# Kernel tuning notes

Hardware: AMD Instinct MI355X
Metric: run time of the kernel (lower is better)

Reference implementation:

```python
import jax, jax.numpy as jnp
import numpy as np

EPS = 1e-5   # BatchNorm3d eps
SLOPE = 0.01 # LeakyReLU default negative_slope

def conv3(x, w, pad):
    return jax.lax.conv_general_dilated(
        x, w, (1, 1, 1), [(pad, pad)] * 3,
        dimension_numbers=('NCDHW', 'OIDHW', 'NCDHW'))

def bn(x):
    # BatchNorm3d in training mode with affine init (weight=1, bias=0):
    # normalize by per-channel batch statistics (biased variance).
    m = x.mean(axis=(0, 2, 3, 4), keepdims=True)
    v = x.var(axis=(0, 2, 3, 4), keepdims=True)
    return (x - m) / jnp.sqrt(v + EPS)

def lrelu(x):
    return jnp.where(x >= 0, x, SLOPE * x)

def block(x, w1, w2):
    # ConvBlock: conv3x3x3 -> BN -> LeakyReLU, twice
    x = lrelu(bn(conv3(x, w1, 1)))
    return lrelu(bn(conv3(x, w2, 1)))

def maxpool2(x):
    # MaxPool3dMPS(kernel=2, stride=2, pad=0) == standard 2x2x2 maxpool
    B, C, D, H, W = x.shape
    return x.reshape(B, C, D // 2, 2, H // 2, 2, W // 2, 2).max(axis=(3, 5, 7))

def upconv_fft(x, w):
    # ConvTranspose3dMPS: nearest-neighbor upsample by stride=2 via repeat,
    # then per-(out,in)-channel CIRCULAR convolution implemented with FFTs
    # (weight zero-padded to the upsampled spatial shape). Vectorized here
    # over all channel pairs with a frequency-domain einsum; rfft is used
    # since all signals are real (identical math, half the memory).
    s = 2
    B, C, D, H, W = x.shape
    up = jnp.broadcast_to(x[:, :, :, None, :, None, :, None],
                          (B, C, D, s, H, s, W, s)).reshape(B, C, D * s, H * s, W * s)
    sp = up.shape[2:]
    X = jnp.fft.rfftn(up, axes=(2, 3, 4))                 # [B, Cin, D', H', Wf]
    Wf = jnp.fft.rfftn(w, s=sp, axes=(2, 3, 4))           # [Cout, Cin, D', H', Wf]
    Y = jnp.einsum('bidhw,oidhw->bodhw', X, Wf)
    return jnp.fft.irfftn(Y, s=sp, axes=(2, 3, 4))

def unet_fwd(x, wf1, wf2, wd1a, wd1b, wd2a, wd2b, wd3a, wd3b,
             wt1, wu1a, wu1b, wt2, wu2a, wu2b, wt3, wu3a, wu3b,
             w_final, b_final):
    x1 = block(x, wf1, wf2)                       # [B,16,64,64,64]
    x2 = block(maxpool2(x1), wd1a, wd1b)          # [B,32,32,32,32]
    x3 = block(maxpool2(x2), wd2a, wd2b)          # [B,64,16,16,16]
    x4 = block(maxpool2(x3), wd3a, wd3b)          # [B,128,8,8,8]

    def up(a, skip, wt, wa, wb):
        u = lrelu(bn(upconv_fft(a, wt)))
        return block(jnp.concatenate([skip, u], axis=1), wa, wb)

    a = up(x4, x3, wt1, wu1a, wu1b)               # [B,64,16,16,16]
    a = up(a, x2, wt2, wu2a, wu2b)                # [B,32,32,32,32]
    a = up(a, x1, wt3, wu3a, wu3b)                # [B,16,64,64,64]
    return conv3(a, w_final, 0) + b_final.reshape(1, -1, 1, 1, 1)

def setup_inputs() -> dict:
    key = jax.random.key(0)
    ks = jax.random.split(key, 32)
    def W(k, shape):
        fan = int(np.prod(shape[1:]))
        return jax.random.normal(k, shape, jnp.float32) * np.float32((2.0 / fan) ** 0.5)
    inp = {}
    inp['x'] = jax.random.normal(ks[0], (1, 1, 64, 64, 64), jnp.float32)
    shapes = {
        'wf1': (16, 1, 3, 3, 3),  'wf2': (16, 16, 3, 3, 3),
        'wd1a': (32, 16, 3, 3, 3), 'wd1b': (32, 32, 3, 3, 3),
        'wd2a': (64, 32, 3, 3, 3), 'wd2b': (64, 64, 3, 3, 3),
        'wd3a': (128, 64, 3, 3, 3), 'wd3b': (128, 128, 3, 3, 3),
        'wt1': (64, 128, 2, 2, 2), 'wu1a': (64, 128, 3, 3, 3), 'wu1b': (64, 64, 3, 3, 3),
        'wt2': (32, 64, 2, 2, 2),  'wu2a': (32, 64, 3, 3, 3),  'wu2b': (32, 32, 3, 3, 3),
        'wt3': (16, 32, 2, 2, 2),  'wu3a': (16, 32, 3, 3, 3),  'wu3b': (16, 16, 3, 3, 3),
        'w_final': (1, 16, 1, 1, 1),
    }
    for i, (name, sh) in enumerate(shapes.items()):
        inp[name] = W(ks[i + 1], sh)
    inp['b_final'] = jnp.zeros((1,), jnp.float32)
    return inp

def reference(x, wf1, wf2, wd1a, wd1b, wd2a, wd2b, wd3a, wd3b,
              wt1, wu1a, wu1b, wt2, wu2a, wu2b, wt3, wu3a, wu3b,
              w_final, b_final):
    return unet_fwd(x, wf1, wf2, wd1a, wd1b, wd2a, wd2b, wd3a, wd3b,
                    wt1, wu1a, wu1b, wt2, wu2a, wu2b, wt3, wu3a, wu3b,
                    w_final, b_final)
```

## Files before the change

### kernel.cpp

```cpp
#include <hip/hip_runtime.h>

#define EPS   1e-5f
#define SLOPE 0.01f

template <int CIN>
__global__ __launch_bounds__(128) void conv3_big(const float* __restrict__ in,
                                                 const float* __restrict__ wt,
                                                 float* __restrict__ out,
                                                 float* __restrict__ bstat) {
    const int V   = 64 * 64 * 64;
    const int NB  = gridDim.y;
    const int co0 = blockIdx.x * 8;
    __shared__ float wlds[27 * CIN * 8];
    __shared__ float tile[3][10][68];
    __shared__ float sred[2 * 16];
    for (int i = threadIdx.x; i < 27 * CIN * 8; i += 128) {
        const int co  = i & 7;
        const int r   = i >> 3;
        const int tap = r % 3;
        const int r2  = r / 3;
        const int pl  = r2 % 9;
        const int ci  = r2 / 9;
        wlds[i] = wt[((size_t)(co0 + co) * CIN + ci) * 27 + pl * 3 + tap];
    }

    const int vb    = blockIdx.y * 512;
    const int d0    = vb >> 12;
    const int hbase = (vb >> 6) & 63;
    const int hh0   = threadIdx.x >> 4;
    const int w0    = (threadIdx.x & 15) * 4;
    const int v0    = vb + (hh0 * 64) + w0;
    const bool mL = (w0 != 0);
    const bool mR = (w0 + 4 != 64);

    int  goff[4];
    int  loff[4];
    bool gok[4];
    bool act[4];
#pragma unroll
    for (int t = 0; t < 4; ++t) {
        const int idx = threadIdx.x + t * 128;
        act[t] = (idx < 480);
        const int r  = idx >> 4;
        const int wq = (idx & 15) * 4;
        const int kd = r / 10;
        const int hh = r - kd * 10;
        const int zd = d0 + kd - 1;
        const int zh = hbase + hh - 1;
        gok[t]  = act[t] & ((unsigned)zd < 64u) & ((unsigned)zh < 64u);
        goff[t] = gok[t] ? ((zd << 6) + zh) * 64 + wq : 0;
        loff[t] = (kd * 10 + hh) * 68 + wq;
    }

    float acc[32];
#pragma unroll
    for (int i = 0; i < 32; ++i) acc[i] = 0.f;

    float4 pre[4];
    {
        const float* pc = in;
#pragma unroll
        for (int t = 0; t < 4; ++t) {
            float4 val = make_float4(0.f, 0.f, 0.f, 0.f);
            if (gok[t]) val = *(const float4*)(pc + goff[t]);
            pre[t] = val;
        }
    }

#pragma unroll 1
    for (int ci = 0; ci < CIN; ++ci) {
        __syncthreads();
#pragma unroll
        for (int t = 0; t < 4; ++t)
            if (act[t]) *(float4*)&((float*)tile)[loff[t]] = pre[t];
        if (ci + 1 < CIN) {
            const float* pc = in + (size_t)(ci + 1) * V;
#pragma unroll
            for (int t = 0; t < 4; ++t) {
                float4 val = make_float4(0.f, 0.f, 0.f, 0.f);
                if (gok[t]) val = *(const float4*)(pc + goff[t]);
                pre[t] = val;
            }
        }
        __syncthreads();
#pragma unroll 1
        for (int kd = 0; kd < 3; ++kd) {
#pragma unroll
            for (int kh = 0; kh < 3; ++kh) {
                const float* trow = &tile[kd][hh0 + kh][0];
                const float4 m = *(const float4*)(trow + w0);
                const float lv = mL ? trow[w0 - 1] : 0.f;
                const float rv = mR ? trow[w0 + 4] : 0.f;
                const float* wb = &wlds[((ci * 9 + kd * 3 + kh) * 3) * 8];
                const float4 t0a = *(const float4*)(wb);
                const float4 t0b = *(const float4*)(wb + 4);
                const float4 t1a = *(const float4*)(wb + 8);
                const float4 t1b = *(const float4*)(wb + 12);
                const float4 t2a = *(const float4*)(wb + 16);
                const float4 t2b = *(const float4*)(wb + 20);
#define FMA4C(A0, A1, A2, AP)                                                       \
                {                                                                   \
                    float* a = (AP);                                                \
                    a[0] = fmaf(lv,  (A0), fmaf(m.x, (A1), fmaf(m.y, (A2), a[0]))); \
                    a[1] = fmaf(m.x, (A0), fmaf(m.y, (A1), fmaf(m.z, (A2), a[1]))); \
                    a[2] = fmaf(m.y, (A0), fmaf(m.z, (A1), fmaf(m.w, (A2), a[2]))); \
                    a[3] = fmaf(m.z, (A0), fmaf(m.w, (A1), fmaf(rv,  (A2), a[3]))); \
                }
                FMA4C(t0a.x, t1a.x, t2a.x, acc + 0);
                FMA4C(t0a.y, t1a.y, t2a.y, acc + 4);
                FMA4C(t0a.z, t1a.z, t2a.z, acc + 8);
                FMA4C(t0a.w, t1a.w, t2a.w, acc + 12);
                FMA4C(t0b.x, t1b.x, t2b.x, acc + 16);
                FMA4C(t0b.y, t1b.y, t2b.y, acc + 20);
                FMA4C(t0b.z, t1b.z, t2b.z, acc + 24);
                FMA4C(t0b.w, t1b.w, t2b.w, acc + 28);
#undef FMA4C
            }
        }
    }
#pragma unroll
    for (int co = 0; co < 8; ++co)
        *(float4*)&out[(size_t)(co0 + co) * V + v0] = *(const float4*)&acc[co * 4];

    float s1[8], s2[8];
#pragma unroll
    for (int co = 0; co < 8; ++co) {
        const float* a = &acc[co * 4];
        s1[co] = a[0] + a[1] + a[2] + a[3];
        s2[co] = fmaf(a[0], a[0], fmaf(a[1], a[1], fmaf(a[2], a[2], a[3] * a[3])));
    }
#pragma unroll
    for (int off = 32; off > 0; off >>= 1)
#pragma unroll
        for (int co = 0; co < 8; ++co) {
            s1[co] += __shfl_down(s1[co], off, 64);
            s2[co] += __shfl_down(s2[co], off, 64);
        }
    const int lane = threadIdx.x & 63;
    const int wv   = threadIdx.x >> 6;
    if (lane == 0)
#pragma unroll
        for (int co = 0; co < 8; ++co) {
            sred[(wv * 8 + co) * 2]     = s1[co];
            sred[(wv * 8 + co) * 2 + 1] = s2[co];
        }
    __syncthreads();
    if ((int)threadIdx.x < 8) {
        float S1 = 0.f, S2 = 0.f;
#pragma unroll
        for (int w = 0; w < 2; ++w) {
            S1 += sred[(w * 8 + threadIdx.x) * 2];
            S2 += sred[(w * 8 + threadIdx.x) * 2 + 1];
        }
        bstat[((size_t)(co0 + threadIdx.x) * NB + blockIdx.y) * 2]     = S1;
        bstat[((size_t)(co0 + threadIdx.x) * NB + blockIdx.y) * 2 + 1] = S2;
    }
}

template <int CIN>
__global__ __launch_bounds__(256) void upconv_big(const float* __restrict__ in,
                                                  const float* __restrict__ wt,
                                                  float* __restrict__ out,
                                                  float* __restrict__ bstat,
                                                  int Di, int Hi, int Wi) {
    const int Do = 2 * Di, Ho = 2 * Hi, Wo = 2 * Wi;
    const int Vo = Do * Ho * Wo;
    const int Vi = Di * Hi * Wi;
    const int NB = gridDim.y;
    const int co0 = blockIdx.x * 8;
    __shared__ float wlds[8 * CIN * 8];
    __shared__ float sred[4 * 16];
    for (int i = threadIdx.x; i < 8 * CIN * 8; i += 256) {
        const int co  = i & 7;
        const int t2  = i >> 3;
        const int ci  = t2 % CIN;
        const int tap = t2 / CIN;
        wlds[i] = wt[((size_t)(co0 + co) * CIN + ci) * 8 + tap];
    }
    __syncthreads();

    const int vbase = blockIdx.y * 1024 + threadIdx.x;
    int od[4], oh[4], ow[4];
#pragma unroll
    for (int j = 0; j < 4; ++j) {
        const int v = vbase + j * 256;
        ow[j] = v % Wo;
        oh[j] = (v / Wo) % Ho;
        od[j] = v / (Wo * Ho);
    }
    float acc[32];
#pragma unroll
    for (int i = 0; i < 32; ++i) acc[i] = 0.f;

#pragma unroll 1
    for (int kd = 0; kd < 2; ++kd)
#pragma unroll 1
    for (int kh = 0; kh < 2; ++kh)
#pragma unroll
    for (int kw = 0; kw < 2; ++kw) {
        const int tap = (kd * 2 + kh) * 2 + kw;
        int sp[4];
#pragma unroll
        for (int j = 0; j < 4; ++j) {
            const int id = ((od[j] - kd + Do) & (Do - 1)) >> 1;
            const int ih = ((oh[j] - kh + Ho) & (Ho - 1)) >> 1;
            const int iw = ((ow[j] - kw + Wo) & (Wo - 1)) >> 1;
            sp[j] = (id * Hi + ih) * Wi + iw;
        }
        const float* wrow = &wlds[tap * CIN * 8];
#pragma unroll 2
        for (int ci = 0; ci < CIN; ++ci) {
            float xv[4];
#pragma unroll
            for (int j = 0; j < 4; ++j)
                xv[j] = in[(size_t)ci * Vi + sp[j]];
            const float4 wa = *(const float4*)(wrow + ci * 8);
            const float4 wb = *(const float4*)(wrow + ci * 8 + 4);
#define UF(WC, CO)                                                              \
            {                                                                   \
                _Pragma("unroll")                                               \
                for (int j = 0; j < 4; ++j)                                     \
                    acc[(CO) * 4 + j] = fmaf(xv[j], (WC), acc[(CO) * 4 + j]);   \
            }
            UF(wa.x, 0) UF(wa.y, 1) UF(wa.z, 2) UF(wa.w, 3)
            UF(wb.x, 4) UF(wb.y, 5) UF(wb.z, 6) UF(wb.w, 7)
#undef UF
        }
    }
#pragma unroll
    for (int co = 0; co < 8; ++co)
#pragma unroll
        for (int j = 0; j < 4; ++j)
            out[(size_t)(co0 + co) * Vo + vbase + j * 256] = acc[co * 4 + j];

    float s1[8], s2[8];
#pragma unroll
    for (int co = 0; co < 8; ++co) {
        const float* a = &acc[co * 4];
        s1[co] = a[0] + a[1] + a[2] + a[3];
        s2[co] = fmaf(a[0], a[0], fmaf(a[1], a[1], fmaf(a[2], a[2], a[3] * a[3])));
    }
#pragma unroll
    for (int off = 32; off > 0; off >>= 1)
#pragma unroll
        for (int co = 0; co < 8; ++co) {
            s1[co] += __shfl_down(s1[co], off, 64);
            s2[co] += __shfl_down(s2[co], off, 64);
        }
    const int lane = threadIdx.x & 63;
    const int wv   = threadIdx.x >> 6;
    if (lane == 0)
#pragma unroll
        for (int co = 0; co < 8; ++co) {
            sred[(wv * 8 + co) * 2]     = s1[co];
            sred[(wv * 8 + co) * 2 + 1] = s2[co];
        }
    __syncthreads();
    if ((int)threadIdx.x < 8) {
        float S1 = 0.f, S2 = 0.f;
#pragma unroll
        for (int w = 0; w < 4; ++w) {
            S1 += sred[(w * 8 + threadIdx.x) * 2];
            S2 += sred[(w * 8 + threadIdx.x) * 2 + 1];
        }
        bstat[((size_t)(co0 + threadIdx.x) * NB + blockIdx.y) * 2]     = S1;
        bstat[((size_t)(co0 + threadIdx.x) * NB + blockIdx.y) * 2 + 1] = S2;
    }
}

__global__ __launch_bounds__(256) void bn_apply_f(const float* __restrict__ prt,
                                                  float* __restrict__ dst,
                                                  const float* __restrict__ bstat,
                                                  int NB, int V4, float invV) {
    const int c = blockIdx.x;
    float s1 = 0.f, s2 = 0.f;
    for (int i = threadIdx.x; i < NB; i += 256) {
        s1 += bstat[((size_t)c * NB + i) * 2];
        s2 += bstat[((size_t)c * NB + i) * 2 + 1];
    }
#pragma unroll
    for (int off = 32; off > 0; off >>= 1) {
        s1 += __shfl_down(s1, off, 64);
        s2 += __shfl_down(s2, off, 64);
    }
    __shared__ float sh[8];
    __shared__ float mv[2];
    const int lane = threadIdx.x & 63;
    const int wv   = threadIdx.x >> 6;
    if (lane == 0) { sh[wv] = s1; sh[4 + wv] = s2; }
    __syncthreads();
    if (threadIdx.x == 0) {
        const float S1 = sh[0] + sh[1] + sh[2] + sh[3];
        const float S2 = sh[4] + sh[5] + sh[6] + sh[7];
        const float mean = S1 * invV;
        const float var  = S2 * invV - mean * mean;
        mv[0] = mean;
        mv[1] = rsqrtf(var + EPS);
    }
    __syncthreads();
    const float mean = mv[0];
    const float rstd = mv[1];
    const int pos = blockIdx.y * 256 + threadIdx.x;
    float4 t = ((const float4*)prt)[(size_t)c * V4 + pos];
    float u;
    u = (t.x - mean) * rstd; t.x = u >= 0.f ? u : SLOPE * u;
    u = (t.y - mean) * rstd; t.y = u >= 0.f ? u : SLOPE * u;
    u = (t.z - mean) * rstd; t.z = u >= 0.f ? u : SLOPE * u;
    u = (t.w - mean) * rstd; t.w = u >= 0.f ? u : SLOPE * u;
    ((float4*)dst)[(size_t)c * V4 + pos] = t;
}

template <int CIN, int CC, int BT>
__global__ __launch_bounds__(BT) void conv3_qA(const float* __restrict__ in,
                                               const float* __restrict__ wt,
                                               float* __restrict__ part,
                                               int D, int H, int W) {
    const int V    = D * H * W;
    const int Cout = gridDim.x * 8;
    const int z    = blockIdx.z;
    const int cib  = z * CC;
    __shared__ float wlds[27 * CC * 8];
    const int co0 = blockIdx.x * 8;
    for (int i = threadIdx.x; i < 27 * CC * 8; i += BT) {
        const int co  = i & 7;
        const int t2  = i >> 3;
        const int tap = t2 % 3;
        const int t3  = t2 / 3;
        const int ci  = t3 % CC;
        const int pl  = t3 / CC;
        wlds[i] = wt[((size_t)(co0 + co) * CIN + cib + ci) * 27 + pl * 3 + tap];
    }
    __syncthreads();

    const float* inz = in + (size_t)cib * V;
    const int v0 = (blockIdx.y * BT + threadIdx.x) * 4;
    const int w0 = v0 % W;
    const int h0 = (v0 / W) % H;
    const int d0 = v0 / (W * H);

    const bool mL = (w0 != 0);
    const bool mR = (w0 + 4 != W);
    const int  wl = w0 - (mL ? 1 : 0);
    const int  wr = w0 + (mR ? 4 : 3);

    float acc[32];
#pragma unroll
    for (int i = 0; i < 32; ++i) acc[i] = 0.f;

#pragma unroll 1
    for (int kd = 0; kd < 3; ++kd) {
#pragma unroll 1
        for (int kh = 0; kh < 3; ++kh) {
            const int zd = d0 + kd - 1, zh = h0 + kh - 1;
            const bool okp = ((unsigned)zd < (unsigned)D) & ((unsigned)zh < (unsigned)H);
            const int row = okp ? (zd * H + zh) * W : 0;
            const float* wpl = &wlds[(kd * 3 + kh) * CC * 24];
#pragma unroll 2
            for (int ci = 0; ci < CC; ++ci) {
                const float* p = inz + (size_t)ci * V + row;
                float4 m = *(const float4*)(p + w0);
                float lv = p[wl];
                float rv = p[wr];
                if (!okp) { m.x = 0.f; m.y = 0.f; m.z = 0.f; m.w = 0.f; }
                if (!(okp && mL)) lv = 0.f;
                if (!(okp && mR)) rv = 0.f;
                const float* wb = wpl + ci * 24;
                const float4 t0a = *(const float4*)(wb);
                const float4 t0b = *(const float4*)(wb + 4);
                const float4 t1a = *(const float4*)(wb + 8);
                const float4 t1b = *(const float4*)(wb + 12);
                const float4 t2a = *(const float4*)(wb + 16);
                const float4 t2b = *(const float4*)(wb + 20);
#define FMA4C(A0, A1, A2, AP)                                                       \
                {                                                                   \
                    float* a = (AP);                                                \
                    a[0] = fmaf(lv,  (A0), fmaf(m.x, (A1), fmaf(m.y, (A2), a[0]))); \
                    a[1] = fmaf(m.x, (A0), fmaf(m.y, (A1), fmaf(m.z, (A2), a[1]))); \
                    a[2] = fmaf(m.y, (A0), fmaf(m.z, (A1), fmaf(m.w, (A2), a[2]))); \
                    a[3] = fmaf(m.z, (A0), fmaf(m.w, (A1), fmaf(rv,  (A2), a[3]))); \
                }
                FMA4C(t0a.x, t1a.x, t2a.x, acc + 0);
                FMA4C(t0a.y, t1a.y, t2a.y, acc + 4);
                FMA4C(t0a.z, t1a.z, t2a.z, acc + 8);
                FMA4C(t0a.w, t1a.w, t2a.w, acc + 12);
                FMA4C(t0b.x, t1b.x, t2b.x, acc + 16);
                FMA4C(t0b.y, t1b.y, t2b.y, acc + 20);
                FMA4C(t0b.z, t1b.z, t2b.z, acc + 24);
                FMA4C(t0b.w, t1b.w, t2b.w, acc + 28);
#undef FMA4C
            }
        }
    }
#pragma unroll
    for (int co = 0; co < 8; ++co)
        *(float4*)&part[((size_t)z * Cout + co0 + co) * V + v0] = *(const float4*)&acc[co * 4];
}

template <int CIN, int CC, int VOXB>
__global__ __launch_bounds__(256) void upconv_v8(const float* __restrict__ in,
                                                 const float* __restrict__ wt,
                                                 float* __restrict__ part,
                                                 int Di, int Hi, int Wi) {
    const int Do = 2 * Di, Ho = 2 * Hi, Wo = 2 * Wi;
    const int Vo = Do * Ho * Wo;
    const int Vi = Di * Hi * Wi;
    const int Cout = gridDim.x * 8;
    const int z    = blockIdx.z;
    const int cib  = z * CC;
    __shared__ float wlds[8 * CC * 8];
    const int co0 = blockIdx.x * 8;
    for (int i = threadIdx.x; i < 8 * CC * 8; i += 256) {
        const int co  = i & 7;
        const int t2  = i >> 3;
        const int ci  = t2 % CC;
        const int tap = t2 / CC;
        wlds[i] = wt[((size_t)(co0 + co) * CIN + cib + ci) * 8 + tap];
    }
    __syncthreads();

    const float* inz = in + (size_t)cib * Vi;
    const int vbase = blockIdx.y * (256 * VOXB) + threadIdx.x;
    int od[VOXB], oh[VOXB], ow[VOXB];
#pragma unroll
    for (int j = 0; j < VOXB; ++j) {
        const int v = vbase + j * 256;
        ow[j] = v % Wo;
        oh[j] = (v / Wo) % Ho;
        od[j] = v / (Wo * Ho);
    }
    float acc[8 * VOXB];
#pragma unroll
    for (int i = 0; i < 8 * VOXB; ++i) acc[i] = 0.f;

#pragma unroll 1
    for (int kd = 0; kd < 2; ++kd)
#pragma unroll 1
    for (int kh = 0; kh < 2; ++kh)
#pragma unroll
    for (int kw = 0; kw < 2; ++kw) {
        const int tap = (kd * 2 + kh) * 2 + kw;
        int sp[VOXB];
#pragma unroll
        for (int j = 0; j < VOXB; ++j) {
            const int id = ((od[j] - kd + Do) & (Do - 1)) >> 1;
            const int ih = ((oh[j] - kh + Ho) & (Ho - 1)) >> 1;
            const int iw = ((ow[j] - kw + Wo) & (Wo - 1)) >> 1;
            sp[j] = (id * Hi + ih) * Wi + iw;
        }
        const float* wrow = &wlds[tap * CC * 8];
#pragma unroll 2
        for (int ci = 0; ci < CC; ++ci) {
            float xv[VOXB];
#pragma unroll
            for (int j = 0; j < VOXB; ++j)
                xv[j] = inz[(size_t)ci * Vi + sp[j]];
            const float4 wa = *(const float4*)(wrow + ci * 8);
            const float4 wb = *(const float4*)(wrow + ci * 8 + 4);
#define UF(WC, CO)                                                              \
            {                                                                   \
                _Pragma("unroll")                                               \
                for (int j = 0; j < VOXB; ++j)                                  \
                    acc[(CO) * VOXB + j] = fmaf(xv[j], (WC), acc[(CO) * VOXB + j]); \
            }
            UF(wa.x, 0) UF(wa.y, 1) UF(wa.z, 2) UF(wa.w, 3)
            UF(wb.x, 4) UF(wb.y, 5) UF(wb.z, 6) UF(wb.w, 7)
#undef UF
        }
    }
#pragma unroll
    for (int co = 0; co < 8; ++co)
#pragma unroll
        for (int j = 0; j < VOXB; ++j)
            part[((size_t)z * Cout + co0 + co) * Vo + vbase + j * 256] = acc[co * VOXB + j];
}

__global__ __launch_bounds__(256) void bn_stats_part_v2(const float* __restrict__ part,
                                                        float* __restrict__ pstat,
                                                        int C, int V, int S, int chunk) {
    const int c = blockIdx.x, seg = blockIdx.y;
    const size_t base = (size_t)c * V + (size_t)seg * chunk;
    float s1 = 0.f, s2 = 0.f;
    for (int i = threadIdx.x * 4; i < chunk; i += 1024) {
        float4 t = make_float4(0.f, 0.f, 0.f, 0.f);
        for (int s = 0; s < S; ++s) {
            const float4 v = *(const float4*)(part + (size_t)s * C * V + base + i);
            t.x += v.x; t.y += v.y; t.z += v.z; t.w += v.w;
        }
        s1 += t.x + t.y + t.z + t.w;
        s2 = fmaf(t.x, t.x, fmaf(t.y, t.y, fmaf(t.z, t.z, fmaf(t.w, t.w, s2))));
    }
#pragma unroll
    for (int off = 32; off > 0; off >>= 1) {
        s1 += __shfl_down(s1, off, 64);
        s2 += __shfl_down(s2, off, 64);
    }
    __shared__ float sh[8];
    const int wid  = threadIdx.x >> 6;
    const int lane = threadIdx.x & 63;
    if (lane == 0) { sh[wid] = s1; sh[4 + wid] = s2; }
    __syncthreads();
    if (threadIdx.x == 0) {
        pstat[(c * gridDim.y + seg) * 2]     = sh[0] + sh[1] + sh[2] + sh[3];
        pstat[(c * gridDim.y + seg) * 2 + 1] = sh[4] + sh[5] + sh[6] + sh[7];
    }
}

__global__ __launch_bounds__(256) void bn_apply_v4(const float* __restrict__ part,
                                                   float* __restrict__ dst,
                                                   const float* __restrict__ pstat,
                                                   int C, int V4, int S, int NSEG,
                                                   float invV, int total4) {
    const int idx = blockIdx.x * blockDim.x + threadIdx.x;
    if (idx >= total4) return;
    const int c = idx / V4;
    const int v = idx - c * V4;
    float s1 = 0.f, s2 = 0.f;
    for (int g = 0; g < NSEG; ++g) {
        s1 += pstat[(c * NSEG + g) * 2];
        s2 += pstat[(c * NSEG + g) * 2 + 1];
    }
    const float mean = s1 * invV;
    const float var  = s2 * invV - mean * mean;
    const float rstd = rsqrtf(var + EPS);
    const float4* p4 = (const float4*)part;
    float4 t = make_float4(0.f, 0.f, 0.f, 0.f);
    for (int s = 0; s < S; ++s) {
        const float4 x = p4[(size_t)(s * C + c) * V4 + v];
        t.x += x.x; t.y += x.y; t.z += x.z; t.w += x.w;
    }
    float u;
    u = (t.x - mean) * rstd; t.x = u >= 0.f ? u : SLOPE * u;
    u = (t.y - mean) * rstd; t.y = u >= 0.f ? u : SLOPE * u;
    u = (t.z - mean) * rstd; t.z = u >= 0.f ? u : SLOPE * u;
    u = (t.w - mean) * rstd; t.w = u >= 0.f ? u : SLOPE * u;
    ((float4*)dst)[idx] = t;
}

__global__ __launch_bounds__(256) void maxpool_kernel(const float* __restrict__ in,
                                                      float* __restrict__ out,
                                                      int D, int H, int W, int total) {
    const int Do = D >> 1, Ho = H >> 1, Wo = W >> 1;
    const int Vo = Do * Ho * Wo;
    const int idx = blockIdx.x * blockDim.x + threadIdx.x;
    if (idx >= total) return;
    const int c  = idx / Vo;
    const int v  = idx - c * Vo;
    const int ow = v % Wo;
    const int oh = (v / Wo) % Ho;
    const int od = v / (Wo * Ho);
    const size_t HW = (size_t)H * W;
    const float* p = in + (size_t)c * D * HW + (size_t)(2 * od) * HW + (size_t)(2 * oh) * W + 2 * ow;
    float m = p[0];
    m = fmaxf(m, p[1]);
    m = fmaxf(m, p[W]);
    m = fmaxf(m, p[W + 1]);
    m = fmaxf(m, p[HW]);
    m = fmaxf(m, p[HW + 1]);
    m = fmaxf(m, p[HW + W]);
    m = fmaxf(m, p[HW + W + 1]);
    out[idx] = m;
}

__global__ __launch_bounds__(256) void final_v2(const float* __restrict__ in,
                                                const float* __restrict__ w,
                                                const float* __restrict__ b,
                                                float* __restrict__ out, int C, int V4) {
    const int idx = blockIdx.x * blockDim.x + threadIdx.x;
    if (idx >= V4) return;
    const float bb = b[0];
    float4 acc = make_float4(bb, bb, bb, bb);
    for (int c = 0; c < C; ++c) {
        const float4 v = ((const float4*)in)[(size_t)c * V4 + idx];
        const float wc = w[c];
        acc.x = fmaf(v.x, wc, acc.x);
        acc.y = fmaf(v.y, wc, acc.y);
        acc.z = fmaf(v.z, wc, acc.z);
        acc.w = fmaf(v.w, wc, acc.w);
    }
    ((float4*)out)[idx] = acc;
}


extern "C" void kernel_launch(void* const* d_in, const int* in_sizes, int n_in,
                              void* d_out, int out_size, void* d_ws, size_t ws_size,
                              hipStream_t stream) {
    const float* x      = (const float*)d_in[0];
    const float* wf1    = (const float*)d_in[1];
    const float* wf2    = (const float*)d_in[2];
    const float* wd1a   = (const float*)d_in[3];
    const float* wd1b   = (const float*)d_in[4];
    const float* wd2a   = (const float*)d_in[5];
    const float* wd2b   = (const float*)d_in[6];
    const float* wd3a   = (const float*)d_in[7];
    const float* wd3b   = (const float*)d_in[8];
    const float* wt1    = (const float*)d_in[9];
    const float* wu1a   = (const float*)d_in[10];
    const float* wu1b   = (const float*)d_in[11];
    const float* wt2    = (const float*)d_in[12];
    const float* wu2a   = (const float*)d_in[13];
    const float* wu2b   = (const float*)d_in[14];
    const float* wt3    = (const float*)d_in[15];
    const float* wu3a   = (const float*)d_in[16];
    const float* wu3b   = (const float*)d_in[17];
    const float* w_fin  = (const float*)d_in[18];
    const float* b_fin  = (const float*)d_in[19];
    float* out = (float*)d_out;

    const int V0 = 64 * 64 * 64;
    const int V1 = 32 * 32 * 32;
    const int V2 = 16 * 16 * 16;
    const int V3 = 8 * 8 * 8;

    float* ws    = (float*)d_ws;
    float* cat3  = ws;
    float* cat2  = cat3 + (size_t)32 * V0;
    float* cat1  = cat2 + (size_t)64 * V1;
    float* x4    = cat1 + (size_t)128 * V2;
    float* tA    = x4   + (size_t)128 * V3;
    float* tB    = tA   + (size_t)16 * V0;
    float* part  = tB   + (size_t)16 * V0;
    float* pstat = part + (size_t)16 * V0;
    float* bstat = pstat + 4096;

    auto blocks = [](int n) { return (n + 255) / 256; };

    auto bn_lrelu = [&](const float* p, float* dstp, int C, int V, int S) {
        const int NSEG = (V >= V0) ? 16 : (V == V1) ? 8 : (V == V2) ? 2 : 1;
        hipLaunchKernelGGL(bn_stats_part_v2, dim3(C, NSEG), dim3(256), 0, stream,
                           p, pstat, C, V, S, V / NSEG);
        const int total4 = C * V / 4;
        hipLaunchKernelGGL(bn_apply_v4, dim3(blocks(total4)), dim3(256), 0, stream,
                           p, dstp, pstat, C, V / 4, S, NSEG, 1.f / V, total4);
    };
    auto maxpool = [&](const float* in, float* o, int C, int D, int H, int W) {
        const int total = C * (D / 2) * (H / 2) * (W / 2);
        hipLaunchKernelGGL(maxpool_kernel, dim3(blocks(total)), dim3(256), 0, stream,
                           in, o, D, H, W, total);
    };

#define CONVBIG(CIN, in_, wt_, prt_, dst_, Cout)                                            \
    {                                                                                       \
        const int NBv = V0 / 512;                                                           \
        dim3 g((Cout) / 8, NBv);                                                            \
        hipLaunchKernelGGL((conv3_big<CIN>), g, dim3(128), 0, stream,                       \
                           in_, wt_, prt_, bstat);                                          \
        hipLaunchKernelGGL(bn_apply_f, dim3(Cout, V0 / 4 / 256), dim3(256), 0, stream,      \
                           prt_, dst_, bstat, NBv, V0 / 4, 1.f / V0);                       \
    }
#define CONVQ(CIN, CC, BT, in_, wt_, prt_, dst_, Cout, D_, H_, W_)                          \
    {                                                                                       \
        const int V_ = (D_) * (H_) * (W_);                                                  \
        const int S  = (CIN) / (CC);                                                        \
        dim3 g((Cout) / 8, V_ / (4 * (BT)), S);                                             \
        hipLaunchKernelGGL((conv3_qA<CIN, CC, BT>), g, dim3(BT), 0, stream,                 \
                           in_, wt_, prt_, D_, H_, W_);                                     \
        bn_lrelu(prt_, dst_, Cout, V_, S);                                                  \
    }
#define UPCONV(CIN, CC, VOXB, in_, wt_, prt_, dst_, Cout, Di_, Hi_, Wi_)                    \
    {                                                                                       \
        const int Vo_ = 8 * (Di_) * (Hi_) * (Wi_);                                          \
        const int S  = (CIN) / (CC);                                                        \
        dim3 g((Cout) / 8, Vo_ / (256 * (VOXB)), S);                                        \
        hipLaunchKernelGGL((upconv_v8<CIN, CC, VOXB>), g, dim3(256), 0, stream,             \
                           in_, wt_, prt_, Di_, Hi_, Wi_);                                  \
        bn_lrelu(prt_, dst_, Cout, Vo_, S);                                                 \
    }

    CONVBIG(1,  x,  wf1, tA, tA,   16);
    CONVBIG(16, tA, wf2, tB, cat3, 16);
    maxpool(cat3, tA, 16, 64, 64, 64);
    CONVQ(16,  8,  64,  tA,  wd1a, part, tB,          32, 32, 32, 32);
    CONVQ(32,  8,  64,  tB,  wd1b, part, cat2,        32, 32, 32, 32);
    maxpool(cat2, tA, 32, 32, 32, 32);
    CONVQ(32,  8,  64,  tA,  wd2a, part, tB,          64, 16, 16, 16);
    CONVQ(64,  8,  64,  tB,  wd2b, part, cat1,        64, 16, 16, 16);
    maxpool(cat1, tA, 64, 16, 16, 16);
    CONVQ(64,  4,  64,  tA,  wd3a, part, tB,         128, 8, 8, 8);
    CONVQ(128, 8,  64,  tB,  wd3b, part, x4,         128, 8, 8, 8);

    UPCONV(128, 16, 1, x4, wt1, part, cat1 + (size_t)64 * V2, 64, 8, 8, 8);
    CONVQ(128, 8,  64, cat1, wu1a, part, tA,          64, 16, 16, 16);
    CONVQ(64,  8,  64, tA,   wu1b, part, tB,          64, 16, 16, 16);

    UPCONV(64, 16, 1, tB, wt2, part, cat2 + (size_t)32 * V1, 32, 16, 16, 16);
    CONVQ(64, 16, 64, cat2, wu2a, part, tA,           32, 32, 32, 32);
    CONVQ(32, 8,  64, tA,   wu2b, part, tB,           32, 32, 32, 32);

    {
        float* up3dst = cat3 + (size_t)16 * V0;
        const int NBv = V0 / 1024;
        dim3 g(2, NBv);
        hipLaunchKernelGGL((upconv_big<32>), g, dim3(256), 0, stream,
                           tB, wt3, up3dst, bstat, 32, 32, 32);
        hipLaunchKernelGGL(bn_apply_f, dim3(16, V0 / 4 / 256), dim3(256), 0, stream,
                           up3dst, up3dst, bstat, NBv, V0 / 4, 1.f / V0);
    }
    CONVBIG(32, cat3, wu3a, tB,   tA, 16);
    CONVBIG(16, tA,   wu3b, cat3, tB, 16);

    hipLaunchKernelGGL(final_v2, dim3(blocks(V0 / 4)), dim3(256), 0, stream,
                       tB, w_fin, b_fin, out, 16, V0 / 4);

#undef CONVBIG
#undef CONVQ
#undef UPCONV
}
```

Measured before the change: 964.3 us.

## Add LDS-tiled 3x3x3 conv kernel for 32^3 layers with register prefetch

```diff
diff --git a/kernel.cpp b/kernel.cpp
--- a/kernel.cpp
+++ b/kernel.cpp
@@ -155,6 +155,124 @@
         bstat[((size_t)(co0 + threadIdx.x) * NB + blockIdx.y) * 2]     = S1;
         bstat[((size_t)(co0 + threadIdx.x) * NB + blockIdx.y) * 2 + 1] = S2;
     }
+}
+
+template <int CIN, int CC>
+__global__ __launch_bounds__(128) void conv3_t32(const float* __restrict__ in,
+                                                 const float* __restrict__ wt,
+                                                 float* __restrict__ part) {
+    const int V    = 32 * 32 * 32;
+    const int Cout = gridDim.x * 8;
+    const int z    = blockIdx.z;
+    const int cib  = z * CC;
+    __shared__ float wlds[27 * CC * 8];
+    __shared__ float tile[3][18][36];
+    const int co0 = blockIdx.x * 8;
+    for (int i = threadIdx.x; i < 27 * CC * 8; i += 128) {
+        const int co  = i & 7;
+        const int r   = i >> 3;
+        const int tap = r % 3;
+        const int r2  = r / 3;
+        const int pl  = r2 % 9;
+        const int ci  = r2 / 9;
+        wlds[i] = wt[((size_t)(co0 + co) * CIN + cib + ci) * 27 + pl * 3 + tap];
+    }
+
+    const int vb    = blockIdx.y * 512;
+    const int d0    = vb >> 10;
+    const int hbase = (vb >> 5) & 31;
+    const int hh0   = threadIdx.x >> 3;
+    const int w0    = (threadIdx.x & 7) * 4;
+    const int v0    = vb + hh0 * 32 + w0;
+    const bool mL = (w0 != 0);
+    const bool mR = (w0 + 4 != 32);
+
+    int  goff[4];
+    int  loff[4];
+    bool gok[4];
+    bool act[4];
+#pragma unroll
+    for (int t = 0; t < 4; ++t) {
+        const int idx = threadIdx.x + t * 128;
+        act[t] = (idx < 432);
+        const int r  = idx >> 3;
+        const int wq = (idx & 7) * 4;
+        const int kd = r / 18;
+        const int hh = r - kd * 18;
+        const int zd = d0 + kd - 1;
+        const int zh = hbase + hh - 1;
+        gok[t]  = act[t] & ((unsigned)zd < 32u) & ((unsigned)zh < 32u);
+        goff[t] = gok[t] ? ((zd << 5) + zh) * 32 + wq : 0;
+        loff[t] = act[t] ? (kd * 18 + hh) * 36 + wq : 0;
+    }
+
+    float acc[32];
+#pragma unroll
+    for (int i = 0; i < 32; ++i) acc[i] = 0.f;
+
+    const float* inz = in + (size_t)cib * V;
+    float4 pre[4];
+#pragma unroll
+    for (int t = 0; t < 4; ++t) {
+        float4 val = make_float4(0.f, 0.f, 0.f, 0.f);
+        if (gok[t]) val = *(const float4*)(inz + goff[t]);
+        pre[t] = val;
+    }
+
+#pragma unroll 1
+    for (int ci = 0; ci < CC; ++ci) {
+        __syncthreads();
+#pragma unroll
+        for (int t = 0; t < 4; ++t)
+            if (act[t]) *(float4*)&((float*)tile)[loff[t]] = pre[t];
+        if (ci + 1 < CC) {
+            const float* pc = inz + (size_t)(ci + 1) * V;
+#pragma unroll
+            for (int t = 0; t < 4; ++t) {
+                float4 val = make_float4(0.f, 0.f, 0.f, 0.f);
+                if (gok[t]) val = *(const float4*)(pc + goff[t]);
+                pre[t] = val;
+            }
+        }
+        __syncthreads();
+#pragma unroll 1
+        for (int kd = 0; kd < 3; ++kd) {
+#pragma unroll
+            for (int kh = 0; kh < 3; ++kh) {
+                const float* trow = &tile[kd][hh0 + kh][0];
+                const float4 m = *(const float4*)(trow + w0);
+                const float lv = mL ? trow[w0 - 1] : 0.f;
+                const float rv = mR ? trow[w0 + 4] : 0.f;
+                const float* wb = &wlds[((ci * 9 + kd * 3 + kh) * 3) * 8];
+                const float4 t0a = *(const float4*)(wb);
+                const float4 t0b = *(const float4*)(wb + 4);
+                const float4 t1a = *(const float4*)(wb + 8);
+                const float4 t1b = *(const float4*)(wb + 12);
+                const float4 t2a = *(const float4*)(wb + 16);
+                const float4 t2b = *(const float4*)(wb + 20);
+#define FMA4C(A0, A1, A2, AP)                                                       \
+                {                                                                   \
+                    float* a = (AP);                                                \
+                    a[0] = fmaf(lv,  (A0), fmaf(m.x, (A1), fmaf(m.y, (A2), a[0]))); \
+                    a[1] = fmaf(m.x, (A0), fmaf(m.y, (A1), fmaf(m.z, (A2), a[1]))); \
+                    a[2] = fmaf(m.y, (A0), fmaf(m.z, (A1), fmaf(m.w, (A2), a[2]))); \
+                    a[3] = fmaf(m.z, (A0), fmaf(m.w, (A1), fmaf(rv,  (A2), a[3]))); \
+                }
+                FMA4C(t0a.x, t1a.x, t2a.x, acc + 0);
+                FMA4C(t0a.y, t1a.y, t2a.y, acc + 4);
+                FMA4C(t0a.z, t1a.z, t2a.z, acc + 8);
+                FMA4C(t0a.w, t1a.w, t2a.w, acc + 12);
+                FMA4C(t0b.x, t1b.x, t2b.x, acc + 16);
+                FMA4C(t0b.y, t1b.y, t2b.y, acc + 20);
+                FMA4C(t0b.z, t1b.z, t2b.z, acc + 24);
+                FMA4C(t0b.w, t1b.w, t2b.w, acc + 28);
+#undef FMA4C
+            }
+        }
+    }
+#pragma unroll
+    for (int co = 0; co < 8; ++co)
+        *(float4*)&part[((size_t)z * Cout + co0 + co) * V + v0] = *(const float4*)&acc[co * 4];
 }
 
 template <int CIN>
@@ -647,6 +765,14 @@
         hipLaunchKernelGGL(bn_apply_f, dim3(Cout, V0 / 4 / 256), dim3(256), 0, stream,      \
                            prt_, dst_, bstat, NBv, V0 / 4, 1.f / V0);                       \
     }
+#define CONVT32(CIN, CC, in_, wt_, prt_, dst_, Cout)                                        \
+    {                                                                                       \
+        const int S = (CIN) / (CC);                                                         \
+        dim3 g((Cout) / 8, V1 / 512, S);                                                    \
+        hipLaunchKernelGGL((conv3_t32<CIN, CC>), g, dim3(128), 0, stream,                   \
+                           in_, wt_, prt_);                                                 \
+        bn_lrelu(prt_, dst_, Cout, V1, S);                                                  \
+    }
 #define CONVQ(CIN, CC, BT, in_, wt_, prt_, dst_, Cout, D_, H_, W_)                          \
     {                                                                                       \
         const int V_ = (D_) * (H_) * (W_);                                                  \
@@ -669,8 +795,8 @@
     CONVBIG(1,  x,  wf1, tA, tA,   16);
     CONVBIG(16, tA, wf2, tB, cat3, 16);
     maxpool(cat3, tA, 16, 64, 64, 64);
-    CONVQ(16,  8,  64,  tA,  wd1a, part, tB,          32, 32, 32, 32);
-    CONVQ(32,  8,  64,  tB,  wd1b, part, cat2,        32, 32, 32, 32);
+    CONVT32(16,  8, tA,  wd1a, part, tB,   32);
+    CONVT32(32,  8, tB,  wd1b, part, cat2, 32);
     maxpool(cat2, tA, 32, 32, 32, 32);
     CONVQ(32,  8,  64,  tA,  wd2a, part, tB,          64, 16, 16, 16);
     CONVQ(64,  8,  64,  tB,  wd2b, part, cat1,        64, 16, 16, 16);
@@ -683,8 +809,8 @@
     CONVQ(64,  8,  64, tA,   wu1b, part, tB,          64, 16, 16, 16);
 
     UPCONV(64, 16, 1, tB, wt2, part, cat2 + (size_t)32 * V1, 32, 16, 16, 16);
-    CONVQ(64, 16, 64, cat2, wu2a, part, tA,           32, 32, 32, 32);
-    CONVQ(32, 8,  64, tA,   wu2b, part, tB,           32, 32, 32, 32);
+    CONVT32(64, 16, cat2, wu2a, part, tA, 32);
+    CONVT32(32, 8,  tA,   wu2b, part, tB, 32);
 
     {
         float* up3dst = cat3 + (size_t)16 * V0;
@@ -702,6 +828,7 @@
                        tB, w_fin, b_fin, out, 16, V0 / 4);
 
 #undef CONVBIG
+#undef CONVT32
 #undef CONVQ
 #undef UPCONV
 }
```

Result: no change. 958.5 us (-0.6%).
